# Kernel optimization log

Measured on AMD Instinct MI355X. Metric: run time of the kernel, lower is better.

Reference implementation:

```python
import jax, jax.numpy as jnp
import numpy as np

N = 100000   # nodes
E = 1000000  # edges (before self-loops)
F = 64       # feat_dim
H = 64       # hidden_dim
G = 512      # graphs in batch
EPS = 1e-5   # BatchNorm1d eps


def setup_inputs() -> dict:
    key = jax.random.key(0)
    ks = jax.random.split(key, 16)
    inp = {}
    inp["x"] = jax.random.normal(ks[0], (N, F), dtype=jnp.float32)
    inp["edge_index"] = jax.random.randint(ks[1], (2, E), 0, N)
    inp["batch"] = jnp.sort(jax.random.randint(ks[2], (N,), 0, G))
    dims = [(F, H), (H, H), (H, H)]
    for i, (di, do) in enumerate(dims):
        # xavier_uniform-scale weights, zero bias (as in weights_init)
        bound = np.sqrt(6.0 / (di + do)).astype(np.float32)
        inp[f"W{i}"] = jax.random.uniform(ks[3 + i], (do, di), dtype=jnp.float32,
                                          minval=-bound, maxval=bound)
        inp[f"b{i}"] = jnp.zeros((do,), dtype=jnp.float32)
        inp[f"g{i}"] = jnp.ones((do,), dtype=jnp.float32)
        inp[f"beta{i}"] = jnp.zeros((do,), dtype=jnp.float32)
    return inp


def reference(x, edge_index, batch,
              W0, b0, g0, beta0,
              W1, b1, g1, beta1,
              W2, b2, g2, beta2):
    # PyG GCNConv: add self-loops, norm = deg^-1/2[src] * deg^-1/2[dst]
    loops = jnp.arange(N)
    src = jnp.concatenate([edge_index[0], loops])  # source j
    dst = jnp.concatenate([edge_index[1], loops])  # target i
    deg = jax.ops.segment_sum(jnp.ones(src.shape, x.dtype), dst, num_segments=N)
    dinv = jnp.where(deg > 0, jax.lax.rsqrt(deg), 0.0)
    norm = dinv[src] * dinv[dst]  # [E+N]

    params = [(W0, b0, g0, beta0), (W1, b1, g1, beta1), (W2, b2, g2, beta2)]
    xs = []
    h = x
    for (W, b, g, beta) in params:
        h = h @ W.T                               # lin (no bias)
        msg = h[src] * norm[:, None]              # gather + scale  [E+N, H]
        h = jax.ops.segment_sum(msg, dst, num_segments=N) + b  # scatter-add + bias
        h = jax.nn.relu(h)
        # BatchNorm1d (training mode: biased batch stats)
        mean = h.mean(axis=0)
        var = h.var(axis=0)
        h = g * (h - mean) * jax.lax.rsqrt(var + EPS) + beta
        xs.append(h)

    # global_add_pool per layer output, then concat
    pooled = [jax.ops.segment_sum(xi, batch, num_segments=G) for xi in xs]
    global_rep = jnp.concatenate(pooled, axis=1)  # [G, 3*H]
    return global_rep, h
```

## Files before the change

### kernel.cpp

```cpp
#include <hip/hip_runtime.h>

#define HD 64
#define BN_EPS 1e-5f

typedef unsigned int u32;
typedef __attribute__((ext_vector_type(8))) short bfrag;
typedef __attribute__((ext_vector_type(4))) float ffrag;

__device__ __forceinline__ unsigned tobf(float x) {
    unsigned u = __float_as_uint(x);
    return (u + 0x7fffu + ((u >> 16) & 1u)) >> 16;
}
__device__ __forceinline__ float bf_lo(unsigned u) { return __uint_as_float(u << 16); }
__device__ __forceinline__ float bf_hi(unsigned u) { return __uint_as_float(u & 0xffff0000u); }


__global__ void k_deg(const int* __restrict__ dst, int* __restrict__ deg, int E) {
    int e = blockIdx.x * blockDim.x + threadIdx.x;
    if (e < E) atomicAdd(&deg[dst[e]], 1);
}

__global__ void k_scan1(const int* __restrict__ deg, int* __restrict__ incl,
                        int* __restrict__ bsums, float* __restrict__ dinv,
                        unsigned* __restrict__ hWs, int N) {
    __shared__ int s[256];
    int tid = threadIdx.x;
    int i = blockIdx.x * 256 + tid;
    if (blockIdx.x == 0 && tid < 32) hWs[(size_t)N * 32 + tid] = 0u;
    int d = (i < N) ? deg[i] : 0;
    int pd = (i < N) ? ((d + 16) & ~15) : 0;
    s[tid] = pd;
    __syncthreads();
    for (int off = 1; off < 256; off <<= 1) {
        int t = (tid >= off) ? s[tid - off] : 0;
        __syncthreads();
        s[tid] += t;
        __syncthreads();
    }
    if (i < N) {
        incl[i] = s[tid];
        dinv[i] = rsqrtf((float)(d + 1));
    }
    if (tid == 255) bsums[blockIdx.x] = s[255];
}

__global__ void k_scan3(int* __restrict__ rowp, const int* __restrict__ deg,
                        const int* __restrict__ incl, const int* __restrict__ bsums,
                        int* __restrict__ ed, int N, int nb) {
    __shared__ float red[256];
    int tid = threadIdx.x;
    int b = blockIdx.x;
    float psum = 0.f;
    for (int t = tid; t < b; t += 256) psum += (float)bsums[t];
    red[tid] = psum;
    __syncthreads();
    for (int off = 128; off > 0; off >>= 1) {
        if (tid < off) red[tid] += red[tid + off];
        __syncthreads();
    }
    int bpre = (int)red[0];
    int i = b * 256 + tid;
    if (i < N) {
        int d = deg[i];
        int pd = (d + 16) & ~15;
        int rv = incl[i] - pd + bpre;
        rowp[i] = rv;
        ed[rv] = i;
        for (int k = d + 1; k < pd; k++) ed[rv + k] = N;
        if (i == N - 1) rowp[N] = rv + pd;
    }
}

__global__ void k_fill(const int* __restrict__ src, const int* __restrict__ dst,
                       const int* __restrict__ rowp, int* __restrict__ cur,
                       int* __restrict__ ed, const int* __restrict__ batch,
                       int* __restrict__ cnt, int E, int N, int G) {
    int e = blockIdx.x * blockDim.x + threadIdx.x;
    if (e < G) {
        int g = e;
        int lo = 0, hi = N;
        while (lo < hi) { int mid = (lo + hi) >> 1; if (batch[mid] < g) lo = mid + 1; else hi = mid; }
        int lo2 = lo, hi2 = N;
        while (lo2 < hi2) { int mid = (lo2 + hi2) >> 1; if (batch[mid] < g + 1) lo2 = mid + 1; else hi2 = mid; }
        cnt[g] = lo2 - lo;
    }
    if (e >= E) return;
    int d = dst[e];
    int pos = rowp[d] + 1 + atomicAdd(&cur[d], 1);
    ed[pos] = src[e];
}

template<int FP32IN>
__global__ __launch_bounds__(256) void k_gemm2(const void* __restrict__ Aptr,
                                               const void* __restrict__ Wptr,
                                               const float* __restrict__ cb,
                                               const float* __restrict__ dinv,
                                               unsigned short* __restrict__ hWs,
                                               int N, int ntiles) {
    int lane = threadIdx.x & 63;
    int m = lane & 15, quad = lane >> 4;
    bfrag wf[4][2];
    if (FP32IN) {
        const float* W = (const float*)Wptr;
#pragma unroll
        for (int ft = 0; ft < 4; ft++)
#pragma unroll
            for (int kf = 0; kf < 2; kf++) {
                const float4* p4 = (const float4*)(W + (ft * 16 + m) * HD + kf * 32 + quad * 8);
                float4 x0 = p4[0], x1 = p4[1];
                union { unsigned u[4]; bfrag b; } r;
                r.u[0] = tobf(x0.x) | (tobf(x0.y) << 16);
                r.u[1] = tobf(x0.z) | (tobf(x0.w) << 16);
                r.u[2] = tobf(x1.x) | (tobf(x1.y) << 16);
                r.u[3] = tobf(x1.z) | (tobf(x1.w) << 16);
                wf[ft][kf] = r.b;
            }
    } else {
        const unsigned short* W = (const unsigned short*)Wptr;
#pragma unroll
        for (int ft = 0; ft < 4; ft++)
#pragma unroll
            for (int kf = 0; kf < 2; kf++)
                wf[ft][kf] = *(const bfrag*)(W + (ft * 16 + m) * HD + kf * 32 + quad * 8);
    }
    float cbv[4];
#pragma unroll
    for (int ft = 0; ft < 4; ft++) cbv[ft] = cb ? cb[ft * 16 + m] : 0.f;

    int wid = (blockIdx.x * blockDim.x + threadIdx.x) >> 6;
    int nw = (gridDim.x * blockDim.x) >> 6;
    for (int tile = wid; tile < ntiles; tile += nw) {
        int arow = min(tile * 16 + m, N - 1);
        bfrag a0, a1;
        if (FP32IN) {
            const float4* p4 = (const float4*)((const float*)Aptr + (size_t)arow * HD + quad * 8);
            float4 x0 = p4[0], x1 = p4[1], y0 = p4[8], y1 = p4[9];
            union { unsigned u[4]; bfrag b; } r0, r1;
            r0.u[0] = tobf(x0.x) | (tobf(x0.y) << 16);
            r0.u[1] = tobf(x0.z) | (tobf(x0.w) << 16);
            r0.u[2] = tobf(x1.x) | (tobf(x1.y) << 16);
            r0.u[3] = tobf(x1.z) | (tobf(x1.w) << 16);
            r1.u[0] = tobf(y0.x) | (tobf(y0.y) << 16);
            r1.u[1] = tobf(y0.z) | (tobf(y0.w) << 16);
            r1.u[2] = tobf(y1.x) | (tobf(y1.y) << 16);
            r1.u[3] = tobf(y1.z) | (tobf(y1.w) << 16);
            a0 = r0.b; a1 = r1.b;
        } else {
            const unsigned short* p = (const unsigned short*)Aptr + (size_t)arow * HD + quad * 8;
            a0 = *(const bfrag*)p;
            a1 = *(const bfrag*)(p + 32);
        }
        ffrag acc[4];
#pragma unroll
        for (int ft = 0; ft < 4; ft++) {
            acc[ft] = (ffrag){0.f, 0.f, 0.f, 0.f};
            acc[ft] = __builtin_amdgcn_mfma_f32_16x16x32_bf16(a0, wf[ft][0], acc[ft], 0, 0, 0);
            acc[ft] = __builtin_amdgcn_mfma_f32_16x16x32_bf16(a1, wf[ft][1], acc[ft], 0, 0, 0);
        }
        int r0n = tile * 16 + quad * 4;
        float dv[4];
#pragma unroll
        for (int r = 0; r < 4; r++) dv[r] = dinv[min(r0n + r, N - 1)];
#pragma unroll
        for (int ft = 0; ft < 4; ft++)
#pragma unroll
            for (int r = 0; r < 4; r++) {
                int nrow = r0n + r;
                if (nrow < N) {
                    float v = (acc[ft][r] + cbv[ft]) * dv[r];
                    hWs[(size_t)nrow * HD + ft * 16 + m] = (unsigned short)tobf(v);
                }
            }
    }
}

__global__ __launch_bounds__(256) void k_agg(const int* __restrict__ rowp,
                                             const int* __restrict__ ed,
                                             const float* __restrict__ dinv,
                                             const unsigned* __restrict__ hWs,
                                             const float* __restrict__ bias,
                                             const int* __restrict__ batch,
                                             void* __restrict__ outp, int outBf,
                                             float* __restrict__ stats,
                                             float* __restrict__ praw,
                                             int N, int chunk,
                                             const float* __restrict__ gam,
                                             const float* __restrict__ bet,
                                             float* __restrict__ ss,
                                             const float* __restrict__ Wnext,
                                             unsigned* __restrict__ Wfb,
                                             float* __restrict__ cf,
                                             float invN, int* __restrict__ ticket) {
    __shared__ u32 sbuf[4][2][1024];
    int tid = threadIdx.x;
    int lane = tid & 63;
    int hf = lane >> 5;
    int m = lane & 31;
    int lsel = lane >> 3;
    int fsel = lane & 7;
    int wv = tid >> 6;
    int wid = blockIdx.x * 4 + wv;
    int i0 = wid * chunk, i1 = min(i0 + chunk, N);
    const uint4* hW4 = (const uint4*)hWs;
    float b0 = bias[2 * m], b1 = bias[2 * m + 1];
    float bs0 = 0.f, bs1 = 0.f, bq0 = 0.f, bq1 = 0.f;
    int curb = -1;
    float p0 = 0.f, p1 = 0.f;
    if (i0 < N) {
        int idx = i0 + lane;
        int rowv = rowp[min(idx, N)];
        float dinvv = dinv[min(idx, N - 1)];
        int batchv = batch[min(idx, N - 1)];
        int s0g = __shfl(rowv, 0);
        int send = __shfl(rowv, i1 - i0);
        int i = i0, ln = 0;
        int rem = (__shfl(rowv, 1) - s0g) >> 4;
        float acc0 = 0.f, acc1 = 0.f;
        int nst = (send - s0g + 31) >> 5;
        int sb = s0g;
        int eidx;
        { int id = sb + m; eidx = (id < send) ? ed[id] : N; }
#pragma unroll
        for (int j = 0; j < 4; j++) {
            int sj = __shfl(eidx, j * 8 + lsel);
            __builtin_amdgcn_global_load_lds(
                (const __attribute__((address_space(1))) u32*)(hW4 + (size_t)sj * 8 + fsel),
                (__attribute__((address_space(3))) u32*)(&sbuf[wv][0][j * 256]),
                16, 0, 0);
        }
        int eidxN = N;
        if (nst > 1) { int id = sb + 32 + m; eidxN = (id < send) ? ed[id] : N; }
        for (int t = 0; t < nst; t++) {
            int cb = t & 1;
            asm volatile("s_waitcnt vmcnt(0)" ::: "memory");
            __builtin_amdgcn_sched_barrier(0);
            if (t + 1 < nst) {
#pragma unroll
                for (int j = 0; j < 4; j++) {
                    int sj = __shfl(eidxN, j * 8 + lsel);
                    __builtin_amdgcn_global_load_lds(
                        (const __attribute__((address_space(1))) u32*)(hW4 + (size_t)sj * 8 + fsel),
                        (__attribute__((address_space(3))) u32*)(&sbuf[wv][cb ^ 1][j * 256]),
                        16, 0, 0);
                }
                if (t + 2 < nst) { int id = sb + 64 + m; eidxN = (id < send) ? ed[id] : N; }
            }
            const u32* cur = &sbuf[wv][cb][0];
            int ng = min(2, (send - sb) >> 4);
            for (int g = 0; g < ng; g++) {
                u32 u[8];
#pragma unroll
                for (int tt = 0; tt < 8; tt++)
                    u[tt] = cur[(g * 16 + hf + 2 * tt) * 32 + m];
#pragma unroll
                for (int tt = 0; tt < 8; tt++) { acc0 += bf_lo(u[tt]); acc1 += bf_hi(u[tt]); }
                if (--rem == 0) {
                    float s0 = acc0 + __shfl_xor(acc0, 32);
                    float s1 = acc1 + __shfl_xor(acc1, 32);
                    float di = __shfl(dinvv, ln);
                    int b = __shfl(batchv, ln);
                    float h0 = fmaxf(fmaf(di, s0, b0), 0.f);
                    float h1 = fmaxf(fmaf(di, s1, b1), 0.f);
                    if (lane < 32) {
                        if (outBf) ((unsigned*)outp)[(size_t)i * 32 + m] = tobf(h0) | (tobf(h1) << 16);
                        else ((float2*)outp)[(size_t)i * 32 + m] = make_float2(h0, h1);
                        bs0 += h0; bs1 += h1;
                        bq0 = fmaf(h0, h0, bq0); bq1 = fmaf(h1, h1, bq1);
                        if (b != curb) {
                            if (curb >= 0) {
                                atomicAdd(&praw[(size_t)curb * HD + 2 * m], p0);
                                atomicAdd(&praw[(size_t)curb * HD + 2 * m + 1], p1);
                            }
                            curb = b; p0 = h0; p1 = h1;
                        } else { p0 += h0; p1 += h1; }
                    }
                    i++; ln++;
                    rem = (i < i1) ? ((__shfl(rowv, ln + 1) - __shfl(rowv, ln)) >> 4)
                                   : 0x3fffffff;
                    acc0 = 0.f; acc1 = 0.f;
                }
            }
            sb += 32;
        }
    }
    if (lane < 32 && curb >= 0) {
        atomicAdd(&praw[(size_t)curb * HD + 2 * m], p0);
        atomicAdd(&praw[(size_t)curb * HD + 2 * m + 1], p1);
    }
    __shared__ float r1s[4][HD], r2s[4][HD];
    if (lane < 32) {
        r1s[wv][2 * m] = bs0; r1s[wv][2 * m + 1] = bs1;
        r2s[wv][2 * m] = bq0; r2s[wv][2 * m + 1] = bq1;
    }
    __syncthreads();
    if (tid < HD) {
        atomicAdd(&stats[tid], r1s[0][tid] + r1s[1][tid] + r1s[2][tid] + r1s[3][tid]);
        atomicAdd(&stats[HD + tid], r2s[0][tid] + r2s[1][tid] + r2s[2][tid] + r2s[3][tid]);
    }
    __shared__ int lastFlag;
    __syncthreads();
    if (tid == 0) {
        __threadfence();
        lastFlag = (atomicAdd(ticket, 1) == (int)gridDim.x - 1) ? 1 : 0;
    }
    __syncthreads();
    if (lastFlag) {
        __shared__ float lss[128];
        __shared__ float cpart[HD][4];
        if (tid < HD) {
            float s1v = atomicAdd(&stats[tid], 0.f);
            float s2v = atomicAdd(&stats[HD + tid], 0.f);
            float mean = s1v * invN;
            float var = s2v * invN - mean * mean;
            float sc = gam[tid] * rsqrtf(var + BN_EPS);
            float sh = bet[tid] - mean * sc;
            ss[tid] = sc; ss[64 + tid] = sh;
            lss[tid] = sc; lss[64 + tid] = sh;
        }
        __syncthreads();
        if (Wnext) {
            int r = tid >> 2, qs = (tid & 3) * 8;
            const float4* W4 = (const float4*)(Wnext + r * HD + 2 * qs);
            float c = 0.f;
#pragma unroll
            for (int t = 0; t < 4; t++) {
                float4 w = W4[t];
                int q = qs + 2 * t;
                Wfb[r * 32 + q]     = tobf(w.x * lss[2 * q])     | (tobf(w.y * lss[2 * q + 1]) << 16);
                Wfb[r * 32 + q + 1] = tobf(w.z * lss[2 * q + 2]) | (tobf(w.w * lss[2 * q + 3]) << 16);
                c = fmaf(lss[64 + 2 * q], w.x, c);
                c = fmaf(lss[64 + 2 * q + 1], w.y, c);
                c = fmaf(lss[64 + 2 * q + 2], w.z, c);
                c = fmaf(lss[64 + 2 * q + 3], w.w, c);
            }
            cpart[r][tid & 3] = c;
            __syncthreads();
            if (tid < HD)
                cf[tid] = cpart[tid][0] + cpart[tid][1] + cpart[tid][2] + cpart[tid][3];
        }
    }
}

__global__ __launch_bounds__(256) void k_fin(float* __restrict__ h,
                                             const float* __restrict__ ss_all,
                                             const float* __restrict__ praw,
                                             const int* __restrict__ cnt,
                                             float* __restrict__ pool,
                                             int nquads, int G) {
    int nb1 = (nquads + 255) >> 8;
    if ((int)blockIdx.x < nb1) {
        int idx = blockIdx.x * 256 + threadIdx.x;
        if (idx >= nquads) return;
        const float* ss = ss_all + 2 * 128;
        float4* h4 = (float4*)h;
        float4 v = h4[idx];
        int f0 = (idx * 4) & 63;
        v.x = fmaf(v.x, ss[f0 + 0], ss[64 + f0 + 0]);
        v.y = fmaf(v.y, ss[f0 + 1], ss[64 + f0 + 1]);
        v.z = fmaf(v.z, ss[f0 + 2], ss[64 + f0 + 2]);
        v.w = fmaf(v.w, ss[f0 + 3], ss[64 + f0 + 3]);
        h4[idx] = v;
    } else {
        int idx = (blockIdx.x - nb1) * 256 + threadIdx.x;
        if (idx >= G * 192) return;
        int g = idx / 192;
        int r = idx - g * 192;
        int l = r >> 6;
        int f = r & 63;
        const float* ss = ss_all + l * 128;
        float v = praw[((size_t)l * G + g) * HD + f];
        pool[idx] = fmaf(ss[f], v, (float)cnt[g] * ss[64 + f]);
    }
}

extern "C" void kernel_launch(void* const* d_in, const int* in_sizes, int n_in,
                              void* d_out, int out_size, void* d_ws, size_t ws_size,
                              hipStream_t stream) {
    const int N = in_sizes[0] / HD;
    const int E = in_sizes[1] / 2;
    const int G = (out_size - N * HD) / 192;

    const float* x = (const float*)d_in[0];
    const int* ei = (const int*)d_in[1];
    const int* srcA = ei;
    const int* dstA = ei + E;
    const int* batch = (const int*)d_in[2];
    const float* W[3]    = {(const float*)d_in[3], (const float*)d_in[7],  (const float*)d_in[11]};
    const float* bias[3] = {(const float*)d_in[4], (const float*)d_in[8],  (const float*)d_in[12]};
    const float* gam[3]  = {(const float*)d_in[5], (const float*)d_in[9],  (const float*)d_in[13]};
    const float* bet[3]  = {(const float*)d_in[6], (const float*)d_in[10], (const float*)d_in[14]};

    char* ws = (char*)d_ws;
    size_t off = 0;
    auto alloc = [&](size_t bytes) -> void* {
        void* p = ws + off;
        off = (off + bytes + 255) & ~(size_t)255;
        return p;
    };
    int* deg     = (int*)alloc((size_t)N * 4);
    int* cur     = (int*)alloc((size_t)N * 4);
    float* stats = (float*)alloc(3 * 128 * 4);
    int* tickets = (int*)alloc(3 * 4);
    float* praw  = (float*)alloc((size_t)3 * G * HD * 4);
    size_t zbytes = off;
    float* dinv  = (float*)alloc((size_t)N * 4);
    int* rowp    = (int*)alloc((size_t)(N + 1) * 4);
    int* incl    = (int*)alloc((size_t)N * 4);
    int* bsums   = (int*)alloc(512 * 4);
    int* ed      = (int*)alloc(((size_t)E + 16 * (size_t)N) * 4 + 512);
    unsigned short* hWs  = (unsigned short*)alloc((size_t)(N + 1) * HD * 2);
    unsigned short* hraw = (unsigned short*)alloc((size_t)N * HD * 2);
    float* ss    = (float*)alloc(3 * 128 * 4);
    unsigned* Wfb = (unsigned*)alloc(2 * HD * 32 * 4);
    float* cf    = (float*)alloc(2 * HD * 4);
    int* gcnt    = (int*)alloc((size_t)G * 4);
    (void)ws_size;

    float* pool = (float*)d_out;
    float* hbuf = (float*)d_out + (size_t)G * 192;

    hipMemsetAsync(deg, 0, zbytes, stream);

    int nb = (N + 255) / 256;
    k_deg<<<(E + 255) / 256, 256, 0, stream>>>(dstA, deg, E);
    k_scan1<<<nb, 256, 0, stream>>>(deg, incl, bsums, dinv, (unsigned*)hWs, N);
    k_scan3<<<nb, 256, 0, stream>>>(rowp, deg, incl, bsums, ed, N, nb);
    k_fill<<<(E + 255) / 256, 256, 0, stream>>>(srcA, dstA, rowp, cur, ed, batch, gcnt, E, N, G);

    const int AGG_BLOCKS = 1024;
    const int NW = AGG_BLOCKS * 4;
    const int chunk = (N + NW - 1) / NW;
    const int ntiles = (N + 15) / 16;

    for (int l = 0; l < 3; l++) {
        if (l == 0)
            k_gemm2<1><<<640, 256, 0, stream>>>(x, W[0], nullptr, dinv, hWs, N, ntiles);
        else
            k_gemm2<0><<<640, 256, 0, stream>>>(hraw, Wfb + (size_t)(l - 1) * HD * 32,
                                                cf + (l - 1) * HD, dinv, hWs, N, ntiles);
        void* outp = (l < 2) ? (void*)hraw : (void*)hbuf;
        k_agg<<<AGG_BLOCKS, 256, 0, stream>>>(rowp, ed, dinv, (const unsigned*)hWs,
                                              bias[l], batch, outp, (l < 2) ? 1 : 0,
                                              stats + l * 128, praw + (size_t)l * G * HD,
                                              N, chunk,
                                              gam[l], bet[l], ss + l * 128,
                                              (l < 2) ? W[l + 1] : nullptr,
                                              Wfb + (size_t)(l < 2 ? l : 0) * HD * 32,
                                              cf + (l < 2 ? l : 0) * HD,
                                              1.0f / (float)N, tickets + l);
    }
    int nquads = N * HD / 4;
    int nb1 = (nquads + 255) / 256;
    int nb2 = (G * 192 + 255) / 256;
    k_fin<<<nb1 + nb2, 256, 0, stream>>>(hbuf, ss, praw, gcnt, pool, nquads, G);
}
```

Baseline: 425.4 us.

## Record edge ranks in degree pass, partition CSR fill, shrink row padding to 8

The degree kernel now saves each edge's atomic rank, so the fill kernel writes edges to their CSR slots without a second atomic counter. The fill kernel is split into 8 partitions over destination-id ranges, each scanning a slab of edges, so writes are localized in cache. Row padding drops from multiples of 16 to 8, cutting the padded gather work in the aggregation kernel, which now reduces in groups of 8 edges. The cost is an extra rank array, each edge slab being read 8 times, and shorter reduction groups.

```diff
diff --git a/kernel.cpp b/kernel.cpp
--- a/kernel.cpp
+++ b/kernel.cpp
@@ -15,9 +15,14 @@
 __device__ __forceinline__ float bf_hi(unsigned u) { return __uint_as_float(u & 0xffff0000u); }
 
 
-__global__ void k_deg(const int* __restrict__ dst, int* __restrict__ deg, int E) {
+__global__ void k_deg(const int* __restrict__ dst, int* __restrict__ deg,
+                      int* __restrict__ rank, int E) {
     int e = blockIdx.x * blockDim.x + threadIdx.x;
-    if (e < E) atomicAdd(&deg[dst[e]], 1);
+    if (e < E) {
+        int d = __builtin_nontemporal_load(&dst[e]);
+        int r = atomicAdd(&deg[d], 1);
+        __builtin_nontemporal_store(r, &rank[e]);
+    }
 }
 
 __global__ void k_scan1(const int* __restrict__ deg, int* __restrict__ incl,
@@ -28,7 +33,7 @@
     int i = blockIdx.x * 256 + tid;
     if (blockIdx.x == 0 && tid < 32) hWs[(size_t)N * 32 + tid] = 0u;
     int d = (i < N) ? deg[i] : 0;
-    int pd = (i < N) ? ((d + 16) & ~15) : 0;
+    int pd = (i < N) ? ((d + 8) & ~7) : 0;
     s[tid] = pd;
     __syncthreads();
     for (int off = 1; off < 256; off <<= 1) {
@@ -62,7 +67,7 @@
     int i = b * 256 + tid;
     if (i < N) {
         int d = deg[i];
-        int pd = (d + 16) & ~15;
+        int pd = (d + 8) & ~7;
         int rv = incl[i] - pd + bpre;
         rowp[i] = rv;
         ed[rv] = i;
@@ -71,23 +76,32 @@
     }
 }
 
+#define FILL_SLAB 4096
 __global__ void k_fill(const int* __restrict__ src, const int* __restrict__ dst,
-                       const int* __restrict__ rowp, int* __restrict__ cur,
+                       const int* __restrict__ rank, const int* __restrict__ rowp,
                        int* __restrict__ ed, const int* __restrict__ batch,
                        int* __restrict__ cnt, int E, int N, int G) {
-    int e = blockIdx.x * blockDim.x + threadIdx.x;
-    if (e < G) {
-        int g = e;
+    int tid = threadIdx.x;
+    int gid = blockIdx.x * 256 + tid;
+    if (gid < G) {
+        int g = gid;
         int lo = 0, hi = N;
         while (lo < hi) { int mid = (lo + hi) >> 1; if (batch[mid] < g) lo = mid + 1; else hi = mid; }
         int lo2 = lo, hi2 = N;
         while (lo2 < hi2) { int mid = (lo2 + hi2) >> 1; if (batch[mid] < g + 1) lo2 = mid + 1; else hi2 = mid; }
         cnt[g] = lo2 - lo;
     }
-    if (e >= E) return;
-    int d = dst[e];
-    int pos = rowp[d] + 1 + atomicAdd(&cur[d], 1);
-    ed[pos] = src[e];
+    int part = blockIdx.x & 7;
+    int base = (blockIdx.x >> 3) * FILL_SLAB;
+    int end = min(base + FILL_SLAB, E);
+    for (int e = base + tid; e < end; e += 256) {
+        int d = __builtin_nontemporal_load(&dst[e]);
+        if (((d >> 12) & 7) == part) {
+            int s = __builtin_nontemporal_load(&src[e]);
+            int r = __builtin_nontemporal_load(&rank[e]);
+            ed[rowp[d] + 1 + r] = s;
+        }
+    }
 }
 
 template<int FP32IN>
@@ -214,12 +228,12 @@
         int s0g = __shfl(rowv, 0);
         int send = __shfl(rowv, i1 - i0);
         int i = i0, ln = 0;
-        int rem = (__shfl(rowv, 1) - s0g) >> 4;
+        int rem = (__shfl(rowv, 1) - s0g) >> 3;
         float acc0 = 0.f, acc1 = 0.f;
         int nst = (send - s0g + 31) >> 5;
         int sb = s0g;
         int eidx;
-        { int id = sb + m; eidx = (id < send) ? ed[id] : N; }
+        { int id = sb + m; eidx = (id < send) ? __builtin_nontemporal_load(&ed[id]) : N; }
 #pragma unroll
         for (int j = 0; j < 4; j++) {
             int sj = __shfl(eidx, j * 8 + lsel);
@@ -229,7 +243,7 @@
                 16, 0, 0);
         }
         int eidxN = N;
-        if (nst > 1) { int id = sb + 32 + m; eidxN = (id < send) ? ed[id] : N; }
+        if (nst > 1) { int id = sb + 32 + m; eidxN = (id < send) ? __builtin_nontemporal_load(&ed[id]) : N; }
         for (int t = 0; t < nst; t++) {
             int cb = t & 1;
             asm volatile("s_waitcnt vmcnt(0)" ::: "memory");
@@ -243,17 +257,17 @@
                         (__attribute__((address_space(3))) u32*)(&sbuf[wv][cb ^ 1][j * 256]),
                         16, 0, 0);
                 }
-                if (t + 2 < nst) { int id = sb + 64 + m; eidxN = (id < send) ? ed[id] : N; }
+                if (t + 2 < nst) { int id = sb + 64 + m; eidxN = (id < send) ? __builtin_nontemporal_load(&ed[id]) : N; }
             }
             const u32* cur = &sbuf[wv][cb][0];
-            int ng = min(2, (send - sb) >> 4);
+            int ng = min(4, (send - sb) >> 3);
             for (int g = 0; g < ng; g++) {
-                u32 u[8];
-#pragma unroll
-                for (int tt = 0; tt < 8; tt++)
-                    u[tt] = cur[(g * 16 + hf + 2 * tt) * 32 + m];
-#pragma unroll
-                for (int tt = 0; tt < 8; tt++) { acc0 += bf_lo(u[tt]); acc1 += bf_hi(u[tt]); }
+                u32 u[4];
+#pragma unroll
+                for (int tt = 0; tt < 4; tt++)
+                    u[tt] = cur[(g * 8 + hf + 2 * tt) * 32 + m];
+#pragma unroll
+                for (int tt = 0; tt < 4; tt++) { acc0 += bf_lo(u[tt]); acc1 += bf_hi(u[tt]); }
                 if (--rem == 0) {
                     float s0 = acc0 + __shfl_xor(acc0, 32);
                     float s1 = acc1 + __shfl_xor(acc1, 32);
@@ -275,7 +289,7 @@
                         } else { p0 += h0; p1 += h1; }
                     }
                     i++; ln++;
-                    rem = (i < i1) ? ((__shfl(rowv, ln + 1) - __shfl(rowv, ln)) >> 4)
+                    rem = (i < i1) ? ((__shfl(rowv, ln + 1) - __shfl(rowv, ln)) >> 3)
                                    : 0x3fffffff;
                     acc0 = 0.f; acc1 = 0.f;
                 }
@@ -398,16 +412,16 @@
         return p;
     };
     int* deg     = (int*)alloc((size_t)N * 4);
-    int* cur     = (int*)alloc((size_t)N * 4);
     float* stats = (float*)alloc(3 * 128 * 4);
     int* tickets = (int*)alloc(3 * 4);
     float* praw  = (float*)alloc((size_t)3 * G * HD * 4);
     size_t zbytes = off;
+    int* rank    = (int*)alloc((size_t)E * 4);
     float* dinv  = (float*)alloc((size_t)N * 4);
     int* rowp    = (int*)alloc((size_t)(N + 1) * 4);
     int* incl    = (int*)alloc((size_t)N * 4);
     int* bsums   = (int*)alloc(512 * 4);
-    int* ed      = (int*)alloc(((size_t)E + 16 * (size_t)N) * 4 + 512);
+    int* ed      = (int*)alloc(((size_t)E + 8 * (size_t)N) * 4 + 512);
     unsigned short* hWs  = (unsigned short*)alloc((size_t)(N + 1) * HD * 2);
     unsigned short* hraw = (unsigned short*)alloc((size_t)N * HD * 2);
     float* ss    = (float*)alloc(3 * 128 * 4);
@@ -422,10 +436,11 @@
     hipMemsetAsync(deg, 0, zbytes, stream);
 
     int nb = (N + 255) / 256;
-    k_deg<<<(E + 255) / 256, 256, 0, stream>>>(dstA, deg, E);
+    k_deg<<<(E + 255) / 256, 256, 0, stream>>>(dstA, deg, rank, E);
     k_scan1<<<nb, 256, 0, stream>>>(deg, incl, bsums, dinv, (unsigned*)hWs, N);
     k_scan3<<<nb, 256, 0, stream>>>(rowp, deg, incl, bsums, ed, N, nb);
-    k_fill<<<(E + 255) / 256, 256, 0, stream>>>(srcA, dstA, rowp, cur, ed, batch, gcnt, E, N, G);
+    int nslab = (E + FILL_SLAB - 1) / FILL_SLAB;
+    k_fill<<<nslab * 8, 256, 0, stream>>>(srcA, dstA, rank, rowp, ed, batch, gcnt, E, N, G);
 
     const int AGG_BLOCKS = 1024;
     const int NW = AGG_BLOCKS * 4;
```

Measured after the change: 416.9 us. 1.02x faster.
